# Kernel tuning notes

Hardware: AMD Instinct MI355X
Metric: run time of the kernel (lower is better)

The kernel has to match this reference:

```python
import jax, jax.numpy as jnp
import numpy as np


def setup_inputs() -> dict:
    key = jax.random.key(0)
    k1, k2, k3 = jax.random.split(key, 3)
    N, D = 8192, 4096
    strength = 1.0
    x = jax.random.normal(k1, (N, D), dtype=jnp.float32)
    cav_raw = jax.random.normal(k2, (D,), dtype=jnp.float32)
    # mirror init: cav = strength * svm_cav / ||svm_cav||
    cav = strength * cav_raw / jnp.sqrt(jnp.sum(cav_raw ** 2))
    bias = jax.random.normal(k3, (D,), dtype=jnp.float32)
    return {"x": x, "cav": cav, "bias": bias}


def reference(x, cav, bias):
    # Original: x_flat - x_flat @ (cav ⊗ cav) + bias @ (cav ⊗ cav), reshaped.
    # (cav ⊗ cav) is rank-1, so the D×D matmul chain collapses to dot products:
    #   x - (x·cav) cav + (bias·cav) cav
    orig_shape = x.shape
    x_flat = x.reshape(x.shape[0], -1)            # [N, D]
    proj = x_flat @ cav                            # [N]  (x_flat @ cav[:,None] squeezed)
    bproj = bias @ cav                             # scalar
    out = x_flat - (proj - bproj)[:, None] * cav[None, :]
    return out.reshape(orig_shape)
```

## Files before the change

### kernel.cpp

```cpp
#include <hip/hip_runtime.h>


#define DIM 4096
#define NTHREADS 256
#define V4_PER_ROW (DIM / 4)
#define V4_PER_THREAD (V4_PER_ROW / NTHREADS)

__global__ void __launch_bounds__(NTHREADS)
svm_bproj_kernel(const float* __restrict__ bias, const float* __restrict__ cav,
                 float* __restrict__ ws) {
    int t = threadIdx.x;
    const float4* b4 = reinterpret_cast<const float4*>(bias);
    const float4* c4 = reinterpret_cast<const float4*>(cav);
    float s = 0.0f;
    #pragma unroll
    for (int k = 0; k < V4_PER_THREAD; ++k) {
        int i = t + k * NTHREADS;
        float4 b = b4[i];
        float4 c = c4[i];
        s += b.x * c.x + b.y * c.y + b.z * c.z + b.w * c.w;
    }
    #pragma unroll
    for (int off = 32; off > 0; off >>= 1) s += __shfl_down(s, off, 64);
    __shared__ float ls[NTHREADS / 64];
    int wave = t >> 6;
    if ((t & 63) == 0) ls[wave] = s;
    __syncthreads();
    if (t == 0) {
        float tot = 0.0f;
        #pragma unroll
        for (int w = 0; w < NTHREADS / 64; ++w) tot += ls[w];
        ws[0] = tot;
    }
}

__global__ void __launch_bounds__(NTHREADS)
svm_proj_kernel(const float* __restrict__ x, const float* __restrict__ cav,
                const float* __restrict__ ws, float* __restrict__ out) {
    const int row = blockIdx.x;
    const int t = threadIdx.x;

    const float4* xr = reinterpret_cast<const float4*>(x + (size_t)row * DIM);
    const float4* c4 = reinterpret_cast<const float4*>(cav);

    float4 xv[V4_PER_THREAD];
    float4 cv[V4_PER_THREAD];
    float s = 0.0f;
    #pragma unroll
    for (int k = 0; k < V4_PER_THREAD; ++k) {
        int i = t + k * NTHREADS;
        xv[k] = xr[i];
        cv[k] = c4[i];
        s += xv[k].x * cv[k].x + xv[k].y * cv[k].y
           + xv[k].z * cv[k].z + xv[k].w * cv[k].w;
    }

    #pragma unroll
    for (int off = 32; off > 0; off >>= 1) s += __shfl_down(s, off, 64);

    __shared__ float ls[NTHREADS / 64];
    int wave = t >> 6;
    if ((t & 63) == 0) ls[wave] = s;
    __syncthreads();

    float proj = 0.0f;
    #pragma unroll
    for (int w = 0; w < NTHREADS / 64; ++w) proj += ls[w];

    const float sc = proj - ws[0];

    float4* orow = reinterpret_cast<float4*>(out + (size_t)row * DIM);
    #pragma unroll
    for (int k = 0; k < V4_PER_THREAD; ++k) {
        int i = t + k * NTHREADS;
        float4 o;
        o.x = xv[k].x - sc * cv[k].x;
        o.y = xv[k].y - sc * cv[k].y;
        o.z = xv[k].z - sc * cv[k].z;
        o.w = xv[k].w - sc * cv[k].w;
        orow[i] = o;
    }
}

extern "C" void kernel_launch(void* const* d_in, const int* in_sizes, int n_in,
                              void* d_out, int out_size, void* d_ws, size_t ws_size,
                              hipStream_t stream) {
    const float* x    = reinterpret_cast<const float*>(d_in[0]);
    const float* cav  = reinterpret_cast<const float*>(d_in[1]);
    const float* bias = reinterpret_cast<const float*>(d_in[2]);
    float* out = reinterpret_cast<float*>(d_out);
    float* ws  = reinterpret_cast<float*>(d_ws);

    const int N = in_sizes[0] / DIM;

    svm_bproj_kernel<<<1, NTHREADS, 0, stream>>>(bias, cav, ws);
    svm_proj_kernel<<<N, NTHREADS, 0, stream>>>(x, cav, ws, out);
}
```

Baseline: 48.44 us.

## Fold bias projection into row kernel and use nontemporal loads/stores

Removes the separate single-block bias·cav kernel by computing (x-bias)·cav per row, so there is one launch and no serial dependency between kernels. Each block now also reads the bias vector, which is small and should stay cached. Loads of x and stores of out become nontemporal to avoid polluting cache with streamed data. The cost is a few extra subtracts and bias loads per block, plus slightly different floating-point rounding.

```diff
diff --git a/kernel.cpp b/kernel.cpp
--- a/kernel.cpp
+++ b/kernel.cpp
@@ -6,79 +6,53 @@
 #define V4_PER_ROW (DIM / 4)
 #define V4_PER_THREAD (V4_PER_ROW / NTHREADS)
 
+typedef float f32x4 __attribute__((ext_vector_type(4)));
+
 __global__ void __launch_bounds__(NTHREADS)
-svm_bproj_kernel(const float* __restrict__ bias, const float* __restrict__ cav,
-                 float* __restrict__ ws) {
-    int t = threadIdx.x;
-    const float4* b4 = reinterpret_cast<const float4*>(bias);
-    const float4* c4 = reinterpret_cast<const float4*>(cav);
+svm_proj_kernel(const float* __restrict__ x, const float* __restrict__ cav,
+                const float* __restrict__ bias, float* __restrict__ out) {
+    const int row = blockIdx.x;
+    const int t = threadIdx.x;
+
+    const f32x4* xr = reinterpret_cast<const f32x4*>(x + (size_t)row * DIM);
+    const f32x4* c4 = reinterpret_cast<const f32x4*>(cav);
+    const f32x4* b4 = reinterpret_cast<const f32x4*>(bias);
+
+    f32x4 xv[V4_PER_THREAD];
+    f32x4 cv[V4_PER_THREAD];
     float s = 0.0f;
     #pragma unroll
     for (int k = 0; k < V4_PER_THREAD; ++k) {
-        int i = t + k * NTHREADS;
-        float4 b = b4[i];
-        float4 c = c4[i];
-        s += b.x * c.x + b.y * c.y + b.z * c.z + b.w * c.w;
-    }
-    #pragma unroll
-    for (int off = 32; off > 0; off >>= 1) s += __shfl_down(s, off, 64);
-    __shared__ float ls[NTHREADS / 64];
-    int wave = t >> 6;
-    if ((t & 63) == 0) ls[wave] = s;
-    __syncthreads();
-    if (t == 0) {
-        float tot = 0.0f;
-        #pragma unroll
-        for (int w = 0; w < NTHREADS / 64; ++w) tot += ls[w];
-        ws[0] = tot;
-    }
-}
-
-__global__ void __launch_bounds__(NTHREADS)
-svm_proj_kernel(const float* __restrict__ x, const float* __restrict__ cav,
-                const float* __restrict__ ws, float* __restrict__ out) {
-    const int row = blockIdx.x;
-    const int t = threadIdx.x;
-
-    const float4* xr = reinterpret_cast<const float4*>(x + (size_t)row * DIM);
-    const float4* c4 = reinterpret_cast<const float4*>(cav);
-
-    float4 xv[V4_PER_THREAD];
-    float4 cv[V4_PER_THREAD];
-    float s = 0.0f;
-    #pragma unroll
-    for (int k = 0; k < V4_PER_THREAD; ++k) {
-        int i = t + k * NTHREADS;
-        xv[k] = xr[i];
+        const int i = t + k * NTHREADS;
+        xv[k] = __builtin_nontemporal_load(&xr[i]);
         cv[k] = c4[i];
-        s += xv[k].x * cv[k].x + xv[k].y * cv[k].y
-           + xv[k].z * cv[k].z + xv[k].w * cv[k].w;
+        const f32x4 b = b4[i];
+        s += (xv[k].x - b.x) * cv[k].x + (xv[k].y - b.y) * cv[k].y
+           + (xv[k].z - b.z) * cv[k].z + (xv[k].w - b.w) * cv[k].w;
     }
 
     #pragma unroll
     for (int off = 32; off > 0; off >>= 1) s += __shfl_down(s, off, 64);
 
     __shared__ float ls[NTHREADS / 64];
-    int wave = t >> 6;
+    const int wave = t >> 6;
     if ((t & 63) == 0) ls[wave] = s;
     __syncthreads();
 
-    float proj = 0.0f;
+    float sc = 0.0f;
     #pragma unroll
-    for (int w = 0; w < NTHREADS / 64; ++w) proj += ls[w];
+    for (int w = 0; w < NTHREADS / 64; ++w) sc += ls[w];
 
-    const float sc = proj - ws[0];
-
-    float4* orow = reinterpret_cast<float4*>(out + (size_t)row * DIM);
+    f32x4* orow = reinterpret_cast<f32x4*>(out + (size_t)row * DIM);
     #pragma unroll
     for (int k = 0; k < V4_PER_THREAD; ++k) {
-        int i = t + k * NTHREADS;
-        float4 o;
+        const int i = t + k * NTHREADS;
+        f32x4 o;
         o.x = xv[k].x - sc * cv[k].x;
         o.y = xv[k].y - sc * cv[k].y;
         o.z = xv[k].z - sc * cv[k].z;
         o.w = xv[k].w - sc * cv[k].w;
-        orow[i] = o;
+        __builtin_nontemporal_store(o, &orow[i]);
     }
 }
 
@@ -89,10 +63,8 @@
     const float* cav  = reinterpret_cast<const float*>(d_in[1]);
     const float* bias = reinterpret_cast<const float*>(d_in[2]);
     float* out = reinterpret_cast<float*>(d_out);
-    float* ws  = reinterpret_cast<float*>(d_ws);
 
     const int N = in_sizes[0] / DIM;
 
-    svm_bproj_kernel<<<1, NTHREADS, 0, stream>>>(bias, cav, ws);
-    svm_proj_kernel<<<N, NTHREADS, 0, stream>>>(x, cav, ws, out);
+    svm_proj_kernel<<<N, NTHREADS, 0, stream>>>(x, cav, bias, out);
 }
```

Result: slower. 53.17 us (+9.8%).
